# Kernel optimization log

Measured on AMD Instinct MI355X. Metric: run time of the kernel, lower is better.

Reference implementation:

```python
import jax, jax.numpy as jnp
import numpy as np

P = 16
IMG_SIZES = [(512, 512), (512, 384), (448, 512), (384, 384), (320, 448), (256, 512), (384, 256), (512, 320)]
LMAX = 1024
B, DIM, HEADS, DH, DEPTH, MLP, NC = 8, 512, 8, 64, 6, 2048, 1000
PD = 3 * P * P  # 768 patch dim


def layer_norm(x, w, b=None, eps=1e-5):
    mu = x.mean(-1, keepdims=True)
    var = ((x - mu) ** 2).mean(-1, keepdims=True)
    y = (x - mu) * jax.lax.rsqrt(var + eps) * w
    return y + b if b is not None else y


def _pack(images):
    # slice each image to its true (static) resolution, patchify, pad to LMAX
    toks, his, wis, msks = [], [], [], []
    for i, (H, W) in enumerate(IMG_SIZES):
        h, w = H // P, W // P
        L = h * w
        img = images[i, :, :H, :W]
        t = img.reshape(3, h, P, w, P).transpose(1, 3, 0, 2, 4).reshape(L, PD)
        hi = jnp.repeat(jnp.arange(h), w)
        wi = jnp.tile(jnp.arange(w), h)
        pad = LMAX - L
        toks.append(jnp.pad(t, ((0, pad), (0, 0))))
        his.append(jnp.pad(hi, (0, pad)))
        wis.append(jnp.pad(wi, (0, pad)))
        msks.append(jnp.arange(LMAX) < L)
    return jnp.stack(toks), jnp.stack(his), jnp.stack(wis), jnp.stack(msks)


def _mha(qx, kx, kmask, wq, wk, wv, qn, kn, wo):
    Bq, Lq, _ = qx.shape
    Lk = kx.shape[1]
    q = (qx @ wq.T).reshape(Bq, Lq, HEADS, DH)
    k = (kx @ wk.T).reshape(Bq, Lk, HEADS, DH)
    v = (kx @ wv.T).reshape(Bq, Lk, HEADS, DH)
    q = layer_norm(q, qn)
    k = layer_norm(k, kn)
    s = jnp.einsum('bqhd,bkhd->bhqk', q, k) / np.sqrt(DH).astype(np.float32)
    s = s + jnp.where(kmask[:, None, None, :], 0.0, -1e9)
    a = jax.nn.softmax(s, axis=-1)
    o = jnp.einsum('bhqk,bkhd->bqhd', a, v).reshape(Bq, Lq, HEADS * DH)
    return o @ wo.T


def setup_inputs() -> dict:
    key = jax.random.key(0)
    ks = iter(jax.random.split(key, 48))

    def nrm(shape, s=0.02):
        return jax.random.normal(next(ks), shape, jnp.float32) * s

    return {
        'images': jax.random.normal(next(ks), (B, 3, 512, 512), jnp.float32),
        'pe_ln1_w': jnp.ones(PD), 'pe_ln1_b': jnp.zeros(PD),
        'pe_w': nrm((DIM, PD)), 'pe_b': jnp.zeros(DIM),
        'pe_ln2_w': jnp.ones(DIM), 'pe_ln2_b': jnp.zeros(DIM),
        'pos_h': nrm((32, DIM), 1.0), 'pos_w': nrm((32, DIM), 1.0),
        'attn_ln': jnp.ones((DEPTH, DIM)),
        'wq': nrm((DEPTH, DIM, DIM)), 'wk': nrm((DEPTH, DIM, DIM)), 'wv': nrm((DEPTH, DIM, DIM)),
        'qn': jnp.ones((DEPTH, DH)), 'kn': jnp.ones((DEPTH, DH)),
        'wo': nrm((DEPTH, DIM, DIM)),
        'ff_ln': jnp.ones((DEPTH, DIM)),
        'ff_w1': nrm((DEPTH, MLP, DIM)), 'ff_b1': jnp.zeros((DEPTH, MLP)),
        'ff_w2': nrm((DEPTH, DIM, MLP)), 'ff_b2': jnp.zeros((DEPTH, DIM)),
        'final_ln': jnp.ones(DIM),
        'pool_q': nrm((DIM,), 1.0), 'pool_ln': jnp.ones(DIM),
        'pool_wq': nrm((DIM, DIM)), 'pool_wk': nrm((DIM, DIM)), 'pool_wv': nrm((DIM, DIM)),
        'pool_qn': jnp.ones(DH), 'pool_kn': jnp.ones(DH),
        'pool_wo': nrm((DIM, DIM)),
        'head_ln': jnp.ones(DIM), 'head_w': nrm((NC, DIM)),
    }


def reference(images, pe_ln1_w, pe_ln1_b, pe_w, pe_b, pe_ln2_w, pe_ln2_b, pos_h, pos_w,
              attn_ln, wq, wk, wv, qn, kn, wo, ff_ln, ff_w1, ff_b1, ff_w2, ff_b2,
              final_ln, pool_q, pool_ln, pool_wq, pool_wk, pool_wv, pool_qn, pool_kn,
              pool_wo, head_ln, head_w):
    tok, hi, wi, mask = _pack(images)
    t = layer_norm(tok, pe_ln1_w, pe_ln1_b)
    t = t @ pe_w.T + pe_b
    t = layer_norm(t, pe_ln2_w, pe_ln2_b)
    t = t + pos_h[hi] + pos_w[wi]
    t = t * mask[..., None]
    for l in range(DEPTH):
        xn = layer_norm(t, attn_ln[l])
        t = t + _mha(xn, xn, mask, wq[l], wk[l], wv[l], qn[l], kn[l], wo[l])
        h = layer_norm(t, ff_ln[l])
        t = t + (jax.nn.gelu(h @ ff_w1[l].T + ff_b1[l], approximate=False) @ ff_w2[l].T + ff_b2[l])
    t = layer_norm(t, final_ln)
    # attention pooling: one learned query per image; context = transformer output (unnormed inside attn)
    q = jnp.broadcast_to(pool_q, (B, 1, DIM))
    qn_ = layer_norm(q, pool_ln)
    pooled = _mha(qn_, t, mask, pool_wq, pool_wk, pool_wv, pool_qn, pool_kn, pool_wo)[:, 0]
    return layer_norm(pooled, head_ln) @ head_w.T
```

## Files before the change

kernel.cpp:

```cpp
#include <hip/hip_runtime.h>
#include <math.h>

#define LMAXS 1024
#define NB 8
#define DIM 512
#define HEADS 8
#define DH 64
#define DEPTH 6
#define MLP 2048
#define NC 1000
#define PDIM 768
#define MPACK 5376
#define MVALID 5360
#define QSCALE 0.18033688f

typedef __attribute__((ext_vector_type(8))) short short8;
typedef __attribute__((ext_vector_type(4))) float floatx4;
typedef unsigned short ushort;

__constant__ int c_w[8]   = {32,24,32,24,28,32,16,20};
__constant__ int c_L[8]   = {1024,768,896,576,560,512,384,640};
__constant__ int c_off[9] = {0,1024,1792,2688,3264,3824,4336,4720,5360};

__device__ __forceinline__ int row2img(int r) {
  int b = 0;
  #pragma unroll
  for (int i = 1; i < 8; ++i) if (r >= c_off[i]) b = i;
  return b;
}

__device__ __forceinline__ ushort f2bf(float x) {
  unsigned int u = __float_as_uint(x);
  u += 0x7fff + ((u >> 16) & 1);
  return (ushort)(u >> 16);
}

#define GLOAD_LDS16(gp, lp) \
  __builtin_amdgcn_global_load_lds((const __attribute__((address_space(1))) void*)(gp), \
                                   (__attribute__((address_space(3))) void*)(lp), 16, 0, 0)

__device__ __forceinline__ void reduce2_256(float& s, float& s2, float* red) {
  #pragma unroll
  for (int off = 32; off; off >>= 1) {
    s  += __shfl_xor(s, off);
    s2 += __shfl_xor(s2, off);
  }
  int wv = threadIdx.x >> 6;
  if ((threadIdx.x & 63) == 0) { red[wv*2] = s; red[wv*2+1] = s2; }
  __syncthreads();
  s  = red[0] + red[2] + red[4] + red[6];
  s2 = red[1] + red[3] + red[5] + red[7];
  __syncthreads();
}

__global__ __launch_bounds__(256) void cvt_k(const float* __restrict__ s, ushort* __restrict__ d, int n) {
  int i = blockIdx.x*256 + threadIdx.x;
  if (i < n) d[i] = f2bf(s[i]);
}
__global__ __launch_bounds__(256) void cvt_qkv_k(
    const float* __restrict__ wq, const float* __restrict__ wk, const float* __restrict__ wv,
    ushort* __restrict__ d) {
  int i = blockIdx.x*256 + threadIdx.x;
  if (i >= 6*1536*512) return;
  int l = i / (1536*512), r = (i / 512) % 1536, k = i & 511;
  const float* src = (r < 512) ? wq : (r < 1024) ? wk : wv;
  int rr = r & 511;
  d[i] = f2bf(src[(size_t)l*DIM*DIM + (size_t)rr*DIM + k]);
}
__global__ __launch_bounds__(256) void cvt_pool_k(
    const float* __restrict__ wk, const float* __restrict__ wv, ushort* __restrict__ d) {
  int i = blockIdx.x*256 + threadIdx.x;
  if (i >= 1024*512) return;
  int r = i >> 9, k = i & 511;
  d[i] = f2bf(r < 512 ? wk[(size_t)r*DIM + k] : wv[(size_t)(r-512)*DIM + k]);
}

__global__ __launch_bounds__(256) void pack_ln1_k(
    const float* __restrict__ images, const float* __restrict__ g,
    const float* __restrict__ bb, ushort* __restrict__ tok) {
  int r = blockIdx.x;
  ushort* out = tok + (size_t)r * PDIM;
  if (r >= MVALID) {
    for (int i = threadIdx.x; i < PDIM; i += 256) out[i] = 0;
    return;
  }
  int b = row2img(r), l = r - c_off[b];
  int wgrid = c_w[b];
  __shared__ float vals[PDIM];
  __shared__ float red[8];
  int hp = l / wgrid, wp = l % wgrid;
  const float* base = images + (size_t)b*3*512*512 + (size_t)hp*16*512 + wp*16;
  float s = 0.f, s2 = 0.f;
  for (int i = threadIdx.x; i < PDIM; i += 256) {
    int c = i >> 8, rr = (i >> 4) & 15, cc = i & 15;
    float v = base[(size_t)c*512*512 + rr*512 + cc];
    vals[i] = v; s += v; s2 += v*v;
  }
  reduce2_256(s, s2, red);
  float mu = s * (1.f/PDIM);
  float rs = rsqrtf(fmaxf(s2*(1.f/PDIM) - mu*mu, 0.f) + 1e-5f);
  for (int i = threadIdx.x; i < PDIM; i += 256)
    out[i] = f2bf((vals[i]-mu)*rs*g[i] + bb[i]);
}

template<int ACT, int OUT>
__global__ __launch_bounds__(256) void gemm_bf(
    const ushort* __restrict__ A, const ushort* __restrict__ W,
    const float* __restrict__ bias, void* __restrict__ Cv,
    int M, int N, int K) {
  __shared__ ushort As[128*64];
  __shared__ ushort Ws[128*64];
  int tid = threadIdx.x;
  int row0 = blockIdx.y*128, col0 = blockIdx.x*128;
  int lane = tid & 63, l15 = lane & 15, quad = lane >> 4;
  int wv = tid >> 6, wm = wv >> 1, wn = wv & 1;
  int sw = l15 & 7;
  int segA = (quad ^ sw) * 8, segB = segA ^ 32;
  const ushort *Ap[4], *Wp[4];
  #pragma unroll
  for (int j = 0; j < 4; ++j) {
    int blk = j*256 + tid;
    int r = blk >> 3, s = ((blk & 7) ^ (r & 7)) * 8;
    Ap[j] = A + (size_t)(row0 + r)*K + s;
    Wp[j] = W + (size_t)(col0 + r)*K + s;
  }
  int ksl = K / gridDim.z;
  int kb0 = blockIdx.z * ksl;
  floatx4 acc[4][4] = {};
  for (int k0 = kb0; k0 < kb0 + ksl; k0 += 64) {
    __syncthreads();
    #pragma unroll
    for (int j = 0; j < 4; ++j) {
      GLOAD_LDS16(Ap[j] + k0, &As[(j*256+tid)*8]);
      GLOAD_LDS16(Wp[j] + k0, &Ws[(j*256+tid)*8]);
    }
    __syncthreads();
    #pragma unroll
    for (int w = 0; w < 2; ++w) {
      int sg = w ? segB : segA;
      short8 af[4], bf[4];
      #pragma unroll
      for (int i = 0; i < 4; ++i) af[i] = *(const short8*)&As[(wm*64 + i*16 + l15)*64 + sg];
      #pragma unroll
      for (int j = 0; j < 4; ++j) bf[j] = *(const short8*)&Ws[(wn*64 + j*16 + l15)*64 + sg];
      #pragma unroll
      for (int i = 0; i < 4; ++i)
        #pragma unroll
        for (int j = 0; j < 4; ++j)
          acc[i][j] = __builtin_amdgcn_mfma_f32_16x16x32_bf16(af[i], bf[j], acc[i][j], 0, 0, 0);
    }
  }
  int rb = row0 + wm*64 + quad*4;
  int cb = col0 + wn*64 + l15;
  bool addb = (bias != nullptr) && (blockIdx.z == 0);
  float* outz = (float*)Cv + (OUT == 3 ? (size_t)blockIdx.z * M * N : 0);
  #pragma unroll
  for (int j = 0; j < 4; ++j) {
    int cc = cb + j*16;
    float bsum = addb ? bias[cc] : 0.f;
    #pragma unroll
    for (int i = 0; i < 4; ++i) {
      int rr = rb + i*16;
      #pragma unroll
      for (int reg = 0; reg < 4; ++reg) {
        float v = acc[i][j][reg] + bsum;
        if (ACT == 1) v = 0.5f*v*(1.f + erff(v*0.70710678118654752f));
        size_t idx = (size_t)(rr + reg)*N + cc;
        if (OUT == 0)      ((float*)Cv)[idx] = v;
        else if (OUT == 3) outz[idx] = v;
        else               ((ushort*)Cv)[idx] = f2bf(v);
      }
    }
  }
}

template<int POOL>
__global__ __launch_bounds__(256) void gemm_qkv_k(
    const ushort* __restrict__ A, const ushort* __restrict__ W,
    const float* __restrict__ gq, const float* __restrict__ gk,
    ushort* __restrict__ Qh, ushort* __restrict__ Kh, ushort* __restrict__ Vh,
    float* __restrict__ KV, int N) {
  const int K = DIM;
  __shared__ ushort As[128*64];
  __shared__ ushort Ws[128*64];
  int tid = threadIdx.x;
  int row0 = blockIdx.y*128, col0 = blockIdx.x*128;
  int lane = tid & 63, l15 = lane & 15, quad = lane >> 4;
  int wv = tid >> 6, wm = wv >> 1, wn = wv & 1;
  int sw = l15 & 7;
  int segA = (quad ^ sw) * 8, segB = segA ^ 32;
  const ushort *Ap[4], *Wp[4];
  #pragma unroll
  for (int j = 0; j < 4; ++j) {
    int blk = j*256 + tid;
    int r = blk >> 3, s = ((blk & 7) ^ (r & 7)) * 8;
    Ap[j] = A + (size_t)(row0 + r)*K + s;
    Wp[j] = W + (size_t)(col0 + r)*K + s;
  }
  floatx4 acc[4][4] = {};
  for (int k0 = 0; k0 < K; k0 += 64) {
    __syncthreads();
    #pragma unroll
    for (int j = 0; j < 4; ++j) {
      GLOAD_LDS16(Ap[j] + k0, &As[(j*256+tid)*8]);
      GLOAD_LDS16(Wp[j] + k0, &Ws[(j*256+tid)*8]);
    }
    __syncthreads();
    #pragma unroll
    for (int w = 0; w < 2; ++w) {
      int sg = w ? segB : segA;
      short8 af[4], bf[4];
      #pragma unroll
      for (int i = 0; i < 4; ++i) af[i] = *(const short8*)&As[(wm*64 + i*16 + l15)*64 + sg];
      #pragma unroll
      for (int j = 0; j < 4; ++j) bf[j] = *(const short8*)&Ws[(wn*64 + j*16 + l15)*64 + sg];
      #pragma unroll
      for (int i = 0; i < 4; ++i)
        #pragma unroll
        for (int j = 0; j < 4; ++j)
          acc[i][j] = __builtin_amdgcn_mfma_f32_16x16x32_bf16(af[i], bf[j], acc[i][j], 0, 0, 0);
    }
  }
  int unit = (col0 >> 6) + wn;
  bool needln = POOL ? (unit < 8) : (unit < 16);
  const float* gain = POOL ? gq : (unit < 8 ? gq : gk);
  #pragma unroll
  for (int i = 0; i < 4; ++i) {
    float s[4] = {0,0,0,0}, s2[4] = {0,0,0,0};
    if (needln) {
      #pragma unroll
      for (int j = 0; j < 4; ++j)
        #pragma unroll
        for (int reg = 0; reg < 4; ++reg) {
          float v = acc[i][j][reg];
          s[reg] += v; s2[reg] += v*v;
        }
      #pragma unroll
      for (int reg = 0; reg < 4; ++reg)
        #pragma unroll
        for (int off = 1; off < 16; off <<= 1) {
          s[reg]  += __shfl_xor(s[reg],  off);
          s2[reg] += __shfl_xor(s2[reg], off);
        }
    }
    #pragma unroll
    for (int reg = 0; reg < 4; ++reg) {
      int r = row0 + wm*64 + i*16 + quad*4 + reg;
      if (r >= MVALID) continue;
      float mu = s[reg]*(1.f/64.f);
      float rs = rsqrtf(fmaxf(s2[reg]*(1.f/64.f) - mu*mu, 0.f) + 1e-5f);
      int b = row2img(r), l = r - c_off[b];
      #pragma unroll
      for (int j = 0; j < 4; ++j) {
        int dh = j*16 + l15;
        float v = acc[i][j][reg];
        if (needln) v = (v - mu)*rs*gain[dh];
        if (POOL) {
          KV[(size_t)r*1024 + unit*64 + dh] = v;
        } else {
          int h = unit & 7;
          size_t dst = ((size_t)(b*8+h)*LMAXS + l)*64 + dh;
          if (unit < 8)       Qh[dst] = f2bf(v * QSCALE);
          else if (unit < 16) Kh[dst] = f2bf(v);
          else                Vh[dst] = f2bf(v);
        }
      }
    }
  }
}

__global__ __launch_bounds__(256) void row_ln_add2_k(
    float* __restrict__ T, const float* __restrict__ P0, const float* __restrict__ P1,
    const float* __restrict__ g, ushort* __restrict__ Y) {
  __shared__ float red[8];
  size_t base = (size_t)blockIdx.x * DIM;
  float v0 = T[base + threadIdx.x], v1 = T[base + threadIdx.x + 256];
  if (P0) {
    v0 += P0[base + threadIdx.x] + P1[base + threadIdx.x];
    v1 += P0[base + threadIdx.x + 256] + P1[base + threadIdx.x + 256];
    T[base + threadIdx.x] = v0;
    T[base + threadIdx.x + 256] = v1;
  }
  float s = v0 + v1, s2 = v0*v0 + v1*v1;
  reduce2_256(s, s2, red);
  float mu = s*(1.f/DIM), rs = rsqrtf(fmaxf(s2*(1.f/DIM) - mu*mu, 0.f) + 1e-5f);
  Y[base + threadIdx.x]       = f2bf((v0-mu)*rs*g[threadIdx.x]);
  Y[base + threadIdx.x + 256] = f2bf((v1-mu)*rs*g[threadIdx.x + 256]);
}

__global__ __launch_bounds__(256) void ln2_pos_k(
    float* __restrict__ T, const float* __restrict__ g, const float* __restrict__ bb,
    const float* __restrict__ ph, const float* __restrict__ pw) {
  int r = blockIdx.x;
  float* x = T + (size_t)r * DIM;
  if (r >= MVALID) {
    for (int i = threadIdx.x; i < DIM; i += 256) x[i] = 0.f;
    return;
  }
  int b = row2img(r), l = r - c_off[b];
  __shared__ float red[8];
  int wgrid = c_w[b];
  int hi = l / wgrid, wi = l % wgrid;
  float s=0.f, s2=0.f;
  for (int i = threadIdx.x; i < DIM; i += 256) { float v = x[i]; s+=v; s2+=v*v; }
  reduce2_256(s, s2, red);
  float mu = s*(1.f/DIM), rs = rsqrtf(fmaxf(s2*(1.f/DIM)-mu*mu, 0.f)+1e-5f);
  for (int i = threadIdx.x; i < DIM; i += 256)
    x[i] = (x[i]-mu)*rs*g[i] + bb[i] + ph[hi*DIM+i] + pw[wi*DIM+i];
}

__global__ __launch_bounds__(256) void vtrans_k(
    const ushort* __restrict__ Vh, ushort* __restrict__ VhT) {
  int bh = blockIdx.x, b = bh >> 3;
  int Lb = c_L[b];
  int lt = blockIdx.y;
  if (lt*64 >= Lb) return;
  __shared__ ushort t[64][72];
  int tid = threadIdx.x;
  int row = tid >> 2, seg = (tid & 3)*16;
  short8 z8 = {};
  if (lt*64 + row < Lb) {
    const ushort* src = Vh + ((size_t)bh*LMAXS + lt*64 + row)*64 + seg;
    *(short8*)&t[row][seg]   = *(const short8*)src;
    *(short8*)&t[row][seg+8] = *(const short8*)(src+8);
  } else {
    *(short8*)&t[row][seg]   = z8;
    *(short8*)&t[row][seg+8] = z8;
  }
  __syncthreads();
  int dh = tid >> 2, ks = (tid & 3)*16;
  short8 o0, o1;
  #pragma unroll
  for (int jj = 0; jj < 8; ++jj) o0[jj] = (short)t[ks+jj][dh];
  #pragma unroll
  for (int jj = 0; jj < 8; ++jj) o1[jj] = (short)t[ks+8+jj][dh];
  ushort* dst = VhT + ((size_t)bh*64 + dh)*LMAXS + lt*64 + ks;
  *(short8*)dst     = o0;
  *(short8*)(dst+8) = o1;
}

__global__ __launch_bounds__(256) void attn_part_k(
    const ushort* __restrict__ Qh, const ushort* __restrict__ Kh,
    const ushort* __restrict__ VhT, float* __restrict__ PART) {
  int bh = blockIdx.x, b = bh >> 3;
  int Lb = c_L[b];
  int qt = blockIdx.y, z = blockIdx.z;
  if (qt*64 >= Lb || z*256 >= Lb) return;
  __shared__ ushort Ks[64*64];
  __shared__ ushort Vt[64*64];
  __shared__ ushort Pb[4][16][68];
  int tid = threadIdx.x, wv = tid >> 6, lane = tid & 63;
  int quad = lane >> 4, l15 = lane & 15;
  int sw = l15 & 7;
  int segA = (quad ^ sw) * 8, segB = segA ^ 32;
  int q0 = qt*64 + wv*16;
  bool active = q0 < Lb;
  const ushort* qhb = Qh + (size_t)bh * LMAXS * DH;
  const ushort* khb = Kh + (size_t)bh * LMAXS * DH;
  const ushort* vtb = VhT + (size_t)bh * DH * LMAXS;
  short8 aq0 = {}, aq1 = {};
  if (active) {
    const ushort* qp = qhb + (size_t)(q0 + l15) * DH;
    aq0 = *(const short8*)(qp + quad*8);
    aq1 = *(const short8*)(qp + 32 + quad*8);
  }
  int blk0 = tid, blk1 = tid + 256;
  int kr0 = blk0 >> 3, s0 = ((blk0 & 7) ^ (kr0 & 7)) * 8;
  int kr1 = blk1 >> 3, s1 = ((blk1 & 7) ^ (kr1 & 7)) * 8;
  const ushort* kg0 = khb + kr0*DH + s0;
  const ushort* kg1 = khb + kr1*DH + s1;
  const ushort* vg0 = vtb + (size_t)kr0*LMAXS + s0;
  const ushort* vg1 = vtb + (size_t)kr1*LMAXS + s1;
  int kbeg = z*256, kend = min(kbeg + 256, Lb);
  float lsum[4] = {0.f,0.f,0.f,0.f};
  floatx4 o[4] = {};
  for (int kc = kbeg; kc < kend; kc += 64) {
    __syncthreads();
    GLOAD_LDS16(kg0 + kc*DH, &Ks[blk0*8]);
    GLOAD_LDS16(kg1 + kc*DH, &Ks[blk1*8]);
    GLOAD_LDS16(vg0 + kc,    &Vt[blk0*8]);
    GLOAD_LDS16(vg1 + kc,    &Vt[blk1*8]);
    __syncthreads();
    if (!active) continue;
    bool tail = (kc + 64 > Lb);
    #pragma unroll
    for (int kb = 0; kb < 4; ++kb) {
      int krow = (kb*16 + l15) * 64;
      floatx4 s = {};
      s = __builtin_amdgcn_mfma_f32_16x16x32_bf16(aq0, *(const short8*)&Ks[krow + segA], s, 0,0,0);
      s = __builtin_amdgcn_mfma_f32_16x16x32_bf16(aq1, *(const short8*)&Ks[krow + segB], s, 0,0,0);
      #pragma unroll
      for (int reg = 0; reg < 4; ++reg) {
        float x = s[reg];
        if (tail && (kc + kb*16 + l15 >= Lb)) x = -1e9f;
        float p = __builtin_amdgcn_exp2f(x);
        lsum[reg] += p;
        Pb[wv][quad*4+reg][kb*16+l15] = f2bf(p);
      }
    }
    short8 a0 = *(const short8*)&Pb[wv][l15][quad*8];
    short8 a1 = *(const short8*)&Pb[wv][l15][32+quad*8];
    #pragma unroll
    for (int nb = 0; nb < 4; ++nb) {
      int vrow = (nb*16 + l15) * 64;
      o[nb] = __builtin_amdgcn_mfma_f32_16x16x32_bf16(a0, *(const short8*)&Vt[vrow + segA], o[nb], 0,0,0);
      o[nb] = __builtin_amdgcn_mfma_f32_16x16x32_bf16(a1, *(const short8*)&Vt[vrow + segB], o[nb], 0,0,0);
    }
  }
  if (active) {
    size_t sb = ((size_t)(bh*16 + qt)*4 + z) * 4160;
    #pragma unroll
    for (int reg = 0; reg < 4; ++reg) {
      float s = lsum[reg];
      s += __shfl_xor(s,1); s += __shfl_xor(s,2); s += __shfl_xor(s,4); s += __shfl_xor(s,8);
      if (l15 == 0) PART[sb + 4096 + wv*16 + quad*4 + reg] = s;
    }
    int rq = wv*16 + quad*4;
    #pragma unroll
    for (int nb = 0; nb < 4; ++nb)
      #pragma unroll
      for (int reg = 0; reg < 4; ++reg)
        PART[sb + (size_t)(rq + reg)*64 + nb*16 + l15] = o[nb][reg];
  }
}

__global__ __launch_bounds__(256) void attn_comb_k(
    const float* __restrict__ PART, ushort* __restrict__ O) {
  int bh = blockIdx.x, b = bh >> 3, h = bh & 7;
  int Lb = c_L[b];
  int qt = blockIdx.y;
  if (qt*64 >= Lb) return;
  int nsl = (Lb + 255) >> 8;
  int t = threadIdx.x;
  int q = t >> 2, dj = (t & 3) * 16;
  int qq = qt*64 + q;
  if (qq >= Lb) return;
  size_t base = (size_t)(bh*16 + qt)*4*4160;
  float o[16] = {};
  float l = 0.f;
  for (int zz = 0; zz < nsl; ++zz) {
    const float* sp = PART + base + (size_t)zz*4160;
    #pragma unroll
    for (int i = 0; i < 16; i += 4) {
      float4 v = *(const float4*)&sp[q*64 + dj + i];
      o[i] += v.x; o[i+1] += v.y; o[i+2] += v.z; o[i+3] += v.w;
    }
    l += sp[4096 + q];
  }
  float inv = 1.f / l;
  short8 r0, r1;
  #pragma unroll
  for (int i = 0; i < 8; ++i) r0[i] = (short)f2bf(o[i]*inv);
  #pragma unroll
  for (int i = 0; i < 8; ++i) r1[i] = (short)f2bf(o[8+i]*inv);
  ushort* dst = O + (size_t)(c_off[b]+qq)*DIM + h*DH + dj;
  *(short8*)dst     = r0;
  *(short8*)(dst+8) = r1;
}

__global__ __launch_bounds__(256) void pool_prep_a_k(
    const float* __restrict__ pq, const float* __restrict__ pln,
    const float* __restrict__ pwq, float* __restrict__ qp) {
  __shared__ float qln[DIM];
  __shared__ float red[8];
  int tid = threadIdx.x;
  float s=0.f, s2=0.f;
  for (int i=tid;i<DIM;i+=256){ float v=pq[i]; s+=v; s2+=v*v; }
  reduce2_256(s, s2, red);
  float mu=s*(1.f/DIM), rs=rsqrtf(fmaxf(s2*(1.f/DIM)-mu*mu,0.f)+1e-5f);
  for (int i=tid;i<DIM;i+=256) qln[i]=(pq[i]-mu)*rs*pln[i];
  __syncthreads();
  int n = blockIdx.x*64 + (tid>>2);
  int kq = (tid&3)*128;
  const float4* wr = (const float4*)(pwq + (size_t)n*DIM + kq);
  float a=0.f;
  #pragma unroll
  for (int k=0;k<32;++k) {
    float4 w4 = wr[k];
    float4 q4 = *(const float4*)&qln[kq + k*4];
    a += w4.x*q4.x + w4.y*q4.y + w4.z*q4.z + w4.w*q4.w;
  }
  a += __shfl_xor(a,1); a += __shfl_xor(a,2);
  if ((tid&3)==0) qp[n]=a;
}

__global__ __launch_bounds__(512) void pool_prep_b_k(
    const float* __restrict__ qp, const float* __restrict__ pqn, float* __restrict__ qpool) {
  int h = threadIdx.x >> 6, lane = threadIdx.x & 63;
  float v = qp[h*64 + lane];
  float s = v, s2 = v*v;
  #pragma unroll
  for (int off=32; off; off>>=1) { s += __shfl_xor(s,off); s2 += __shfl_xor(s2,off); }
  float mu = s*(1.f/64), rs = rsqrtf(fmaxf(s2*(1.f/64)-mu*mu, 0.f)+1e-5f);
  qpool[h*64+lane] = (v-mu)*rs*pqn[lane];
}

__global__ __launch_bounds__(256) void pool_attn_part_k(
    const float* __restrict__ qpool, const float* __restrict__ KV,
    float* __restrict__ PARTP) {
  __shared__ float qh[DH];
  __shared__ float ps[256];
  __shared__ float op[4][DH];
  __shared__ float red[8];
  int bh = blockIdx.x, c = blockIdx.y;
  int b = bh>>3, h = bh&7;
  int Lb = c_L[b];
  int tid = threadIdx.x;
  if (tid < DH) qh[tid] = qpool[h*DH + tid];
  __syncthreads();
  int kk = c*256 + tid;
  float p = 0.f;
  if (kk < Lb) {
    const float4* kp = (const float4*)(KV + (size_t)(c_off[b]+kk)*1024 + h*DH);
    float a = 0.f;
    #pragma unroll
    for (int dd=0; dd<16; ++dd) {
      float4 kv = kp[dd];
      a += kv.x*qh[dd*4] + kv.y*qh[dd*4+1] + kv.z*qh[dd*4+2] + kv.w*qh[dd*4+3];
    }
    p = __expf(a*0.125f);
  }
  ps[tid] = p;
  float s = p, s2 = 0.f;
  reduce2_256(s, s2, red);
  int wvv = tid >> 6, lane = tid & 63;
  float o = 0.f;
  int kb = c*256 + wvv*64;
  const float* vb = KV + (size_t)c_off[b]*1024 + 512 + h*DH + lane;
  for (int j = 0; j < 64; ++j) {
    int key = kb + j;
    if (key < Lb) o += ps[wvv*64+j] * vb[(size_t)key*1024];
  }
  op[wvv][lane] = o;
  __syncthreads();
  if (tid < DH)
    PARTP[((size_t)bh*4 + c)*66 + tid] = op[0][tid]+op[1][tid]+op[2][tid]+op[3][tid];
  if (tid == 64)
    PARTP[((size_t)bh*4 + c)*66 + 64] = s;
}

__global__ __launch_bounds__(64) void pool_attn_comb_k(
    const float* __restrict__ PARTP, float* __restrict__ O) {
  int bh = blockIdx.x, b = bh>>3, h = bh&7, d = threadIdx.x;
  float o = 0.f, sum = 0.f;
  #pragma unroll
  for (int c = 0; c < 4; ++c) {
    o   += PARTP[((size_t)bh*4 + c)*66 + d];
    sum += PARTP[((size_t)bh*4 + c)*66 + 64];
  }
  O[(size_t)b*DIM + h*DH + d] = o / sum;
}

__global__ __launch_bounds__(256) void proj512_k(
    const float* __restrict__ X, const float* __restrict__ W, float* __restrict__ Y) {
  __shared__ float xr[DIM];
  int b = blockIdx.x, tid = threadIdx.x;
  for (int i=tid;i<DIM;i+=256) xr[i] = X[(size_t)b*DIM+i];
  __syncthreads();
  if (tid < 128) {
    int n = blockIdx.y*128 + tid;
    const float4* wr = (const float4*)(W + (size_t)n*DIM);
    float a=0.f;
    for (int k=0;k<DIM/4;++k) { float4 w4 = wr[k]; a += w4.x*xr[k*4]+w4.y*xr[k*4+1]+w4.z*xr[k*4+2]+w4.w*xr[k*4+3]; }
    Y[(size_t)b*DIM+n]=a;
  }
}

__global__ __launch_bounds__(256) void head_out_k(
    const float* __restrict__ X, const float* __restrict__ g,
    const float* __restrict__ W, float* __restrict__ out) {
  __shared__ float xr[DIM];
  __shared__ float red[8];
  int b = blockIdx.x, tid = threadIdx.x;
  float s=0.f, s2=0.f;
  for (int i=tid;i<DIM;i+=256){ float v=X[(size_t)b*DIM+i]; s+=v; s2+=v*v; }
  reduce2_256(s, s2, red);
  float mu=s*(1.f/DIM), rs=rsqrtf(fmaxf(s2*(1.f/DIM)-mu*mu,0.f)+1e-5f);
  for (int i=tid;i<DIM;i+=256) xr[i]=(X[(size_t)b*DIM+i]-mu)*rs*g[i];
  __syncthreads();
  if (tid < 125) {
    int n = blockIdx.y*125 + tid;
    const float4* wr = (const float4*)(W + (size_t)n*DIM);
    float a=0.f;
    for (int k=0;k<DIM/4;++k){ float4 w4=wr[k]; a += w4.x*xr[k*4]+w4.y*xr[k*4+1]+w4.z*xr[k*4+2]+w4.w*xr[k*4+3]; }
    out[(size_t)b*NC+n]=a;
  }
}

extern "C" void kernel_launch(void* const* d_in, const int* in_sizes, int n_in,
                              void* d_out, int out_size, void* d_ws, size_t ws_size,
                              hipStream_t stream) {
  const float* images  = (const float*)d_in[0];
  const float* pe_ln1_w= (const float*)d_in[1];
  const float* pe_ln1_b= (const float*)d_in[2];
  const float* pe_w    = (const float*)d_in[3];
  const float* pe_b    = (const float*)d_in[4];
  const float* pe_ln2_w= (const float*)d_in[5];
  const float* pe_ln2_b= (const float*)d_in[6];
  const float* pos_h   = (const float*)d_in[7];
  const float* pos_w   = (const float*)d_in[8];
  const float* attn_ln = (const float*)d_in[9];
  const float* wq      = (const float*)d_in[10];
  const float* wk      = (const float*)d_in[11];
  const float* wvp     = (const float*)d_in[12];
  const float* qn      = (const float*)d_in[13];
  const float* kn      = (const float*)d_in[14];
  const float* wo      = (const float*)d_in[15];
  const float* ff_ln   = (const float*)d_in[16];
  const float* ff_w1   = (const float*)d_in[17];
  const float* ff_b1   = (const float*)d_in[18];
  const float* ff_w2   = (const float*)d_in[19];
  const float* ff_b2   = (const float*)d_in[20];
  const float* final_ln= (const float*)d_in[21];
  const float* pool_q  = (const float*)d_in[22];
  const float* pool_ln = (const float*)d_in[23];
  const float* pool_wq = (const float*)d_in[24];
  const float* pool_wk = (const float*)d_in[25];
  const float* pool_wv = (const float*)d_in[26];
  const float* pool_qn = (const float*)d_in[27];
  const float* pool_kn = (const float*)d_in[28];
  const float* pool_wo = (const float*)d_in[29];
  const float* head_ln = (const float*)d_in[30];
  const float* head_w  = (const float*)d_in[31];
  (void)ws_size; (void)in_sizes; (void)n_in; (void)out_size;

  char* p = (char*)d_ws;
  ushort* WQKVc = (ushort*)p; p += (size_t)6*1536*512*2;
  ushort* WOc   = (ushort*)p; p += (size_t)6*512*512*2;
  ushort* W1c   = (ushort*)p; p += (size_t)6*2048*512*2;
  ushort* W2c   = (ushort*)p; p += (size_t)6*512*2048*2;
  ushort* PEWc  = (ushort*)p; p += (size_t)512*768*2;
  ushort* PKVc  = (ushort*)p; p += (size_t)1024*512*2;
  float*  T     = (float*)p;  p += (size_t)MPACK*DIM*4;
  ushort* Qh    = (ushort*)p; p += (size_t)64*LMAXS*DH*2;
  ushort* Kh    = (ushort*)p; p += (size_t)64*LMAXS*DH*2;
  ushort* VhT   = (ushort*)p; p += (size_t)64*64*LMAXS*2;
  ushort* FFH   = (ushort*)p; p += (size_t)MPACK*MLP*2;
  ushort* TOK   = FFH;
  ushort* ATTO  = FFH;
  char*   R     = p;          p += (size_t)64*16*4*4160*4;
  float*  PART  = (float*)R;
  float*  P0    = (float*)R;
  float*  P1    = (float*)(R + (size_t)MPACK*DIM*4);
  ushort* XN    = (ushort*)(R + (size_t)2*MPACK*DIM*4);
  ushort* Vh    = (ushort*)(R + (size_t)2*MPACK*DIM*4 + (size_t)MPACK*DIM*2);
  float*  KVb   = (float*)R;
  float*  QP    = (float*)p;  p += DIM*4;
  float*  QPOOL = (float*)p;  p += DIM*4;
  float*  POOLO = (float*)p;  p += NB*DIM*4;
  float*  POOLED= (float*)p;  p += NB*DIM*4;
  float*  PARTP = (float*)p;  p += (size_t)64*4*66*4;

  cvt_qkv_k<<<(6*1536*512+255)/256, 256, 0, stream>>>(wq, wk, wvp, WQKVc);
  cvt_k<<<(6*512*512+255)/256, 256, 0, stream>>>(wo, WOc, 6*512*512);
  cvt_k<<<(6*2048*512+255)/256, 256, 0, stream>>>(ff_w1, W1c, 6*2048*512);
  cvt_k<<<(6*512*2048+255)/256, 256, 0, stream>>>(ff_w2, W2c, 6*512*2048);
  cvt_k<<<(512*768+255)/256, 256, 0, stream>>>(pe_w, PEWc, 512*768);
  cvt_pool_k<<<(1024*512+255)/256, 256, 0, stream>>>(pool_wk, pool_wv, PKVc);

  pack_ln1_k<<<MPACK, 256, 0, stream>>>(images, pe_ln1_w, pe_ln1_b, TOK);
  gemm_bf<0,0><<<dim3(4, MPACK/128), 256, 0, stream>>>(TOK, PEWc, pe_b, T, MPACK, DIM, PDIM);
  ln2_pos_k<<<MPACK, 256, 0, stream>>>(T, pe_ln2_w, pe_ln2_b, pos_h, pos_w);

  for (int l = 0; l < DEPTH; ++l) {
    row_ln_add2_k<<<MPACK, 256, 0, stream>>>(T, l ? P0 : nullptr, P1, attn_ln + l*DIM, XN);
    gemm_qkv_k<0><<<dim3(12, MPACK/128), 256, 0, stream>>>(
        XN, WQKVc + (size_t)l*1536*512, qn + l*DH, kn + l*DH, Qh, Kh, Vh, nullptr, 1536);
    vtrans_k<<<dim3(64, 16), 256, 0, stream>>>(Vh, VhT);
    attn_part_k<<<dim3(64, 16, 4), 256, 0, stream>>>(Qh, Kh, VhT, PART);
    attn_comb_k<<<dim3(64, 16), 256, 0, stream>>>(PART, ATTO);
    gemm_bf<0,3><<<dim3(4, MPACK/128, 2), 256, 0, stream>>>(ATTO, WOc + (size_t)l*512*512, nullptr, P0, MPACK, DIM, DIM);
    row_ln_add2_k<<<MPACK, 256, 0, stream>>>(T, P0, P1, ff_ln + l*DIM, XN);
    gemm_bf<1,2><<<dim3(16, MPACK/128), 256, 0, stream>>>(XN, W1c + (size_t)l*MLP*DIM, ff_b1 + l*MLP, FFH, MPACK, MLP, DIM);
    gemm_bf<0,3><<<dim3(4, MPACK/128, 2), 256, 0, stream>>>(FFH, W2c + (size_t)l*DIM*MLP, ff_b2 + l*DIM, P0, MPACK, DIM, MLP);
  }

  row_ln_add2_k<<<MPACK, 256, 0, stream>>>(T, P0, P1, final_ln, XN);
  pool_prep_a_k<<<8, 256, 0, stream>>>(pool_q, pool_ln, pool_wq, QP);
  pool_prep_b_k<<<1, 512, 0, stream>>>(QP, pool_qn, QPOOL);
  gemm_qkv_k<1><<<dim3(8, MPACK/128), 256, 0, stream>>>(
      XN, PKVc, pool_kn, nullptr, nullptr, nullptr, nullptr, KVb, 1024);
  pool_attn_part_k<<<dim3(64, 4), 256, 0, stream>>>(QPOOL, KVb, PARTP);
  pool_attn_comb_k<<<64, 64, 0, stream>>>(PARTP, POOLO);
  proj512_k<<<dim3(8, 4), 256, 0, stream>>>(POOLO, pool_wo, POOLED);
  head_out_k<<<dim3(8, 8), 256, 0, stream>>>(POOLED, head_ln, head_w, (float*)d_out);
}
```

Baseline: 1.293 ms.

## Fuse residual add into GEMM epilogues, retile GEMMs, halve attention key splits

Templates the GEMM on tile and wave shapes and uses smaller tiles (64x128, 64x64) to raise block counts. It drops split-K for the output and FFN2 projections and has them accumulate straight into the residual stream T. The separate add-and-LayerNorm kernel becomes a plain LayerNorm, which removes the P0/P1 partial buffers and their extra reads and writes. Attention now splits keys into 2 chunks of 512 instead of 4 of 256, cutting partial-buffer traffic at the cost of less parallelism and a longer per-block loop.

```diff
diff --git a/kernel.cpp b/kernel.cpp
--- a/kernel.cpp
+++ b/kernel.cpp
@@ -103,63 +103,67 @@
     out[i] = f2bf((vals[i]-mu)*rs*g[i] + bb[i]);
 }
 
-template<int ACT, int OUT>
-__global__ __launch_bounds__(256) void gemm_bf(
+template<int TM, int TN, int WM, int WN, int ACT, int OUT>
+__global__ __launch_bounds__(256) void gemm_t(
     const ushort* __restrict__ A, const ushort* __restrict__ W,
     const float* __restrict__ bias, void* __restrict__ Cv,
     int M, int N, int K) {
-  __shared__ ushort As[128*64];
-  __shared__ ushort Ws[128*64];
+  constexpr int WAVES_N = TN / WN;
+  constexpr int FM = WM / 16, FN = WN / 16;
+  constexpr int NA = TM / 32, NW = TN / 32;
+  __shared__ ushort As[TM*64];
+  __shared__ ushort Ws[TN*64];
   int tid = threadIdx.x;
-  int row0 = blockIdx.y*128, col0 = blockIdx.x*128;
+  int row0 = blockIdx.y*TM, col0 = blockIdx.x*TN;
   int lane = tid & 63, l15 = lane & 15, quad = lane >> 4;
-  int wv = tid >> 6, wm = wv >> 1, wn = wv & 1;
+  int wv = tid >> 6;
+  int wm = wv / WAVES_N, wn = wv % WAVES_N;
   int sw = l15 & 7;
   int segA = (quad ^ sw) * 8, segB = segA ^ 32;
-  const ushort *Ap[4], *Wp[4];
-  #pragma unroll
-  for (int j = 0; j < 4; ++j) {
+  const ushort *Ap[NA], *Wp[NW];
+  #pragma unroll
+  for (int j = 0; j < NA; ++j) {
     int blk = j*256 + tid;
     int r = blk >> 3, s = ((blk & 7) ^ (r & 7)) * 8;
     Ap[j] = A + (size_t)(row0 + r)*K + s;
+  }
+  #pragma unroll
+  for (int j = 0; j < NW; ++j) {
+    int blk = j*256 + tid;
+    int r = blk >> 3, s = ((blk & 7) ^ (r & 7)) * 8;
     Wp[j] = W + (size_t)(col0 + r)*K + s;
   }
-  int ksl = K / gridDim.z;
-  int kb0 = blockIdx.z * ksl;
-  floatx4 acc[4][4] = {};
-  for (int k0 = kb0; k0 < kb0 + ksl; k0 += 64) {
+  floatx4 acc[FM][FN] = {};
+  for (int k0 = 0; k0 < K; k0 += 64) {
     __syncthreads();
     #pragma unroll
-    for (int j = 0; j < 4; ++j) {
-      GLOAD_LDS16(Ap[j] + k0, &As[(j*256+tid)*8]);
-      GLOAD_LDS16(Wp[j] + k0, &Ws[(j*256+tid)*8]);
-    }
+    for (int j = 0; j < NA; ++j) GLOAD_LDS16(Ap[j] + k0, &As[(j*256+tid)*8]);
+    #pragma unroll
+    for (int j = 0; j < NW; ++j) GLOAD_LDS16(Wp[j] + k0, &Ws[(j*256+tid)*8]);
     __syncthreads();
     #pragma unroll
     for (int w = 0; w < 2; ++w) {
       int sg = w ? segB : segA;
-      short8 af[4], bf[4];
-      #pragma unroll
-      for (int i = 0; i < 4; ++i) af[i] = *(const short8*)&As[(wm*64 + i*16 + l15)*64 + sg];
-      #pragma unroll
-      for (int j = 0; j < 4; ++j) bf[j] = *(const short8*)&Ws[(wn*64 + j*16 + l15)*64 + sg];
-      #pragma unroll
-      for (int i = 0; i < 4; ++i)
+      short8 af[FM], bf[FN];
+      #pragma unroll
+      for (int i = 0; i < FM; ++i) af[i] = *(const short8*)&As[(wm*WM + i*16 + l15)*64 + sg];
+      #pragma unroll
+      for (int j = 0; j < FN; ++j) bf[j] = *(const short8*)&Ws[(wn*WN + j*16 + l15)*64 + sg];
+      #pragma unroll
+      for (int i = 0; i < FM; ++i)
         #pragma unroll
-        for (int j = 0; j < 4; ++j)
+        for (int j = 0; j < FN; ++j)
           acc[i][j] = __builtin_amdgcn_mfma_f32_16x16x32_bf16(af[i], bf[j], acc[i][j], 0, 0, 0);
     }
   }
-  int rb = row0 + wm*64 + quad*4;
-  int cb = col0 + wn*64 + l15;
-  bool addb = (bias != nullptr) && (blockIdx.z == 0);
-  float* outz = (float*)Cv + (OUT == 3 ? (size_t)blockIdx.z * M * N : 0);
-  #pragma unroll
-  for (int j = 0; j < 4; ++j) {
+  int rb = row0 + wm*WM + quad*4;
+  int cb = col0 + wn*WN + l15;
+  #pragma unroll
+  for (int j = 0; j < FN; ++j) {
     int cc = cb + j*16;
-    float bsum = addb ? bias[cc] : 0.f;
-    #pragma unroll
-    for (int i = 0; i < 4; ++i) {
+    float bsum = bias ? bias[cc] : 0.f;
+    #pragma unroll
+    for (int i = 0; i < FM; ++i) {
       int rr = rb + i*16;
       #pragma unroll
       for (int reg = 0; reg < 4; ++reg) {
@@ -167,7 +171,7 @@
         if (ACT == 1) v = 0.5f*v*(1.f + erff(v*0.70710678118654752f));
         size_t idx = (size_t)(rr + reg)*N + cc;
         if (OUT == 0)      ((float*)Cv)[idx] = v;
-        else if (OUT == 3) outz[idx] = v;
+        else if (OUT == 1) ((float*)Cv)[idx] += v;
         else               ((ushort*)Cv)[idx] = f2bf(v);
       }
     }
@@ -269,18 +273,11 @@
   }
 }
 
-__global__ __launch_bounds__(256) void row_ln_add2_k(
-    float* __restrict__ T, const float* __restrict__ P0, const float* __restrict__ P1,
-    const float* __restrict__ g, ushort* __restrict__ Y) {
+__global__ __launch_bounds__(256) void row_ln_bf_k(
+    const float* __restrict__ T, const float* __restrict__ g, ushort* __restrict__ Y) {
   __shared__ float red[8];
   size_t base = (size_t)blockIdx.x * DIM;
   float v0 = T[base + threadIdx.x], v1 = T[base + threadIdx.x + 256];
-  if (P0) {
-    v0 += P0[base + threadIdx.x] + P1[base + threadIdx.x];
-    v1 += P0[base + threadIdx.x + 256] + P1[base + threadIdx.x + 256];
-    T[base + threadIdx.x] = v0;
-    T[base + threadIdx.x + 256] = v1;
-  }
   float s = v0 + v1, s2 = v0*v0 + v1*v1;
   reduce2_256(s, s2, red);
   float mu = s*(1.f/DIM), rs = rsqrtf(fmaxf(s2*(1.f/DIM) - mu*mu, 0.f) + 1e-5f);
@@ -345,7 +342,7 @@
   int bh = blockIdx.x, b = bh >> 3;
   int Lb = c_L[b];
   int qt = blockIdx.y, z = blockIdx.z;
-  if (qt*64 >= Lb || z*256 >= Lb) return;
+  if (qt*64 >= Lb || z*512 >= Lb) return;
   __shared__ ushort Ks[64*64];
   __shared__ ushort Vt[64*64];
   __shared__ ushort Pb[4][16][68];
@@ -371,7 +368,7 @@
   const ushort* kg1 = khb + kr1*DH + s1;
   const ushort* vg0 = vtb + (size_t)kr0*LMAXS + s0;
   const ushort* vg1 = vtb + (size_t)kr1*LMAXS + s1;
-  int kbeg = z*256, kend = min(kbeg + 256, Lb);
+  int kbeg = z*512, kend = min(kbeg + 512, Lb);
   float lsum[4] = {0.f,0.f,0.f,0.f};
   floatx4 o[4] = {};
   for (int kc = kbeg; kc < kend; kc += 64) {
@@ -408,7 +405,7 @@
     }
   }
   if (active) {
-    size_t sb = ((size_t)(bh*16 + qt)*4 + z) * 4160;
+    size_t sb = ((size_t)(bh*16 + qt)*2 + z) * 4160;
     #pragma unroll
     for (int reg = 0; reg < 4; ++reg) {
       float s = lsum[reg];
@@ -430,12 +427,12 @@
   int Lb = c_L[b];
   int qt = blockIdx.y;
   if (qt*64 >= Lb) return;
-  int nsl = (Lb + 255) >> 8;
+  int nsl = (Lb + 511) >> 9;
   int t = threadIdx.x;
   int q = t >> 2, dj = (t & 3) * 16;
   int qq = qt*64 + q;
   if (qq >= Lb) return;
-  size_t base = (size_t)(bh*16 + qt)*4*4160;
+  size_t base = (size_t)(bh*16 + qt)*2*4160;
   float o[16] = {};
   float l = 0.f;
   for (int zz = 0; zz < nsl; ++zz) {
@@ -632,19 +629,16 @@
   ushort* PEWc  = (ushort*)p; p += (size_t)512*768*2;
   ushort* PKVc  = (ushort*)p; p += (size_t)1024*512*2;
   float*  T     = (float*)p;  p += (size_t)MPACK*DIM*4;
+  ushort* XN    = (ushort*)p; p += (size_t)MPACK*DIM*2;
   ushort* Qh    = (ushort*)p; p += (size_t)64*LMAXS*DH*2;
   ushort* Kh    = (ushort*)p; p += (size_t)64*LMAXS*DH*2;
+  ushort* Vh    = (ushort*)p; p += (size_t)64*LMAXS*DH*2;
   ushort* VhT   = (ushort*)p; p += (size_t)64*64*LMAXS*2;
   ushort* FFH   = (ushort*)p; p += (size_t)MPACK*MLP*2;
   ushort* TOK   = FFH;
   ushort* ATTO  = FFH;
-  char*   R     = p;          p += (size_t)64*16*4*4160*4;
-  float*  PART  = (float*)R;
-  float*  P0    = (float*)R;
-  float*  P1    = (float*)(R + (size_t)MPACK*DIM*4);
-  ushort* XN    = (ushort*)(R + (size_t)2*MPACK*DIM*4);
-  ushort* Vh    = (ushort*)(R + (size_t)2*MPACK*DIM*4 + (size_t)MPACK*DIM*2);
-  float*  KVb   = (float*)R;
+  float*  PART  = (float*)p;  p += (size_t)64*16*2*4160*4;
+  float*  KVb   = (float*)p;  p += (size_t)MPACK*1024*4;
   float*  QP    = (float*)p;  p += DIM*4;
   float*  QPOOL = (float*)p;  p += DIM*4;
   float*  POOLO = (float*)p;  p += NB*DIM*4;
@@ -659,23 +653,23 @@
   cvt_pool_k<<<(1024*512+255)/256, 256, 0, stream>>>(pool_wk, pool_wv, PKVc);
 
   pack_ln1_k<<<MPACK, 256, 0, stream>>>(images, pe_ln1_w, pe_ln1_b, TOK);
-  gemm_bf<0,0><<<dim3(4, MPACK/128), 256, 0, stream>>>(TOK, PEWc, pe_b, T, MPACK, DIM, PDIM);
+  gemm_t<64,128,64,32,0,0><<<dim3(4, MPACK/64), 256, 0, stream>>>(TOK, PEWc, pe_b, T, MPACK, DIM, PDIM);
   ln2_pos_k<<<MPACK, 256, 0, stream>>>(T, pe_ln2_w, pe_ln2_b, pos_h, pos_w);
 
   for (int l = 0; l < DEPTH; ++l) {
-    row_ln_add2_k<<<MPACK, 256, 0, stream>>>(T, l ? P0 : nullptr, P1, attn_ln + l*DIM, XN);
+    row_ln_bf_k<<<MPACK, 256, 0, stream>>>(T, attn_ln + l*DIM, XN);
     gemm_qkv_k<0><<<dim3(12, MPACK/128), 256, 0, stream>>>(
         XN, WQKVc + (size_t)l*1536*512, qn + l*DH, kn + l*DH, Qh, Kh, Vh, nullptr, 1536);
     vtrans_k<<<dim3(64, 16), 256, 0, stream>>>(Vh, VhT);
-    attn_part_k<<<dim3(64, 16, 4), 256, 0, stream>>>(Qh, Kh, VhT, PART);
+    attn_part_k<<<dim3(64, 16, 2), 256, 0, stream>>>(Qh, Kh, VhT, PART);
     attn_comb_k<<<dim3(64, 16), 256, 0, stream>>>(PART, ATTO);
-    gemm_bf<0,3><<<dim3(4, MPACK/128, 2), 256, 0, stream>>>(ATTO, WOc + (size_t)l*512*512, nullptr, P0, MPACK, DIM, DIM);
-    row_ln_add2_k<<<MPACK, 256, 0, stream>>>(T, P0, P1, ff_ln + l*DIM, XN);
-    gemm_bf<1,2><<<dim3(16, MPACK/128), 256, 0, stream>>>(XN, W1c + (size_t)l*MLP*DIM, ff_b1 + l*MLP, FFH, MPACK, MLP, DIM);
-    gemm_bf<0,3><<<dim3(4, MPACK/128, 2), 256, 0, stream>>>(FFH, W2c + (size_t)l*DIM*MLP, ff_b2 + l*DIM, P0, MPACK, DIM, MLP);
-  }
-
-  row_ln_add2_k<<<MPACK, 256, 0, stream>>>(T, P0, P1, final_ln, XN);
+    gemm_t<64,64,32,32,0,1><<<dim3(8, MPACK/64), 256, 0, stream>>>(ATTO, WOc + (size_t)l*512*512, nullptr, T, MPACK, DIM, DIM);
+    row_ln_bf_k<<<MPACK, 256, 0, stream>>>(T, ff_ln + l*DIM, XN);
+    gemm_t<64,128,64,32,1,2><<<dim3(16, MPACK/64), 256, 0, stream>>>(XN, W1c + (size_t)l*MLP*DIM, ff_b1 + l*MLP, FFH, MPACK, MLP, DIM);
+    gemm_t<64,64,32,32,0,1><<<dim3(8, MPACK/64), 256, 0, stream>>>(FFH, W2c + (size_t)l*DIM*MLP, ff_b2 + l*DIM, T, MPACK, DIM, MLP);
+  }
+
+  row_ln_bf_k<<<MPACK, 256, 0, stream>>>(T, final_ln, XN);
   pool_prep_a_k<<<8, 256, 0, stream>>>(pool_q, pool_ln, pool_wq, QP);
   pool_prep_b_k<<<1, 512, 0, stream>>>(QP, pool_qn, QPOOL);
   gemm_qkv_k<1><<<dim3(8, MPACK/128), 256, 0, stream>>>(
```

After: 1.240 ms. 4.1% less time.
